# Kernel tuning notes

Hardware: AMD Instinct MI355X
Metric: run time of the kernel (lower is better)

## Reference

```python
import jax, jax.numpy as jnp
import numpy as np

N = 50000      # nodes
E = 500000     # edges
F_IN = 128     # num_features
H = 128        # hidden_dim
G = 256        # graphs in batch


def setup_inputs() -> dict:
    key = jax.random.key(0)
    ks = jax.random.split(key, 12)
    x = jax.random.normal(ks[0], (N, F_IN), jnp.float32)
    edge_index = jax.random.randint(ks[1], (2, E), 0, N, dtype=jnp.int32)
    edge_attr = jax.random.uniform(ks[2], (E,), jnp.float32)  # positive edge weights
    batch = jnp.sort(jax.random.randint(ks[3], (N,), 0, G, dtype=jnp.int32))
    s_in = 1.0 / np.sqrt(F_IN)
    s_h = 1.0 / np.sqrt(H)
    return {
        "x": x,
        "edge_index": edge_index,
        "edge_attr": edge_attr,
        "batch": batch,
        "W1": jax.random.normal(ks[4], (H, F_IN), jnp.float32) * s_in,
        "b1": jnp.zeros((H,), jnp.float32),
        "W2": jax.random.normal(ks[5], (H, H), jnp.float32) * s_h,
        "b2": jnp.zeros((H,), jnp.float32),
        "fW1": jax.random.normal(ks[6], (H, H), jnp.float32) * s_h,
        "fb1": jnp.zeros((H,), jnp.float32),
        "fW2": jax.random.normal(ks[7], (1, H), jnp.float32) * s_h,
        "fb2": jnp.zeros((1,), jnp.float32),
    }


def gcn_conv(x, src, dst, ew, W, b, n):
    """PyG GCNConv: linear transform, add self-loops (weight 1),
    symmetric deg^-1/2 normalization with edge weights, scatter-add, bias."""
    h = x @ W.T                                   # [n, H]
    loop = jnp.arange(n, dtype=src.dtype)
    s = jnp.concatenate([src, loop])
    d = jnp.concatenate([dst, loop])
    w = jnp.concatenate([ew, jnp.ones((n,), x.dtype)])
    deg = jax.ops.segment_sum(w, d, num_segments=n)  # weighted in-degree incl. self-loop
    dinv = jnp.where(deg > 0, jax.lax.rsqrt(deg), 0.0)
    norm = dinv[s] * w * dinv[d]                  # [E+n]
    msg = h[s] * norm[:, None]                    # gather + scale: [E+n, H]
    out = jax.ops.segment_sum(msg, d, num_segments=n)  # scatter-add
    return out + b


def reference(x, edge_index, edge_attr, batch, W1, b1, W2, b2, fW1, fb1, fW2, fb2):
    src, dst = edge_index[0], edge_index[1]
    h = jax.nn.relu(gcn_conv(x, src, dst, edge_attr, W1, b1, N))
    h = jax.nn.relu(gcn_conv(h, src, dst, edge_attr, W2, b2, N))
    # global_mean_pool over graph ids
    sums = jax.ops.segment_sum(h, batch, num_segments=G)            # [G, H]
    counts = jax.ops.segment_sum(jnp.ones((N,), h.dtype), batch, num_segments=G)
    pooled = sums / jnp.maximum(counts, 1.0)[:, None]
    o = jax.nn.relu(pooled @ fW1.T + fb1)
    return o @ fW2.T + fb2                                          # [G, 1]
```

## Files before the change

kernel.cpp:

```cpp
#include <hip/hip_runtime.h>
#include <hip/hip_bf16.h>


#define CAP 64
#define CDS 8

typedef __attribute__((ext_vector_type(8))) short short8;
typedef __attribute__((ext_vector_type(4))) float floatx4;

__device__ inline unsigned short f2bf(float f) {
    unsigned int u = __float_as_uint(f);
    u += 0x7FFF + ((u >> 16) & 1);
    return (unsigned short)(u >> 16);
}
__device__ inline float bf2f(unsigned short h) {
    return __uint_as_float(((unsigned int)h) << 16);
}

#define PW 136
__global__ __launch_bounds__(256) void gemm1_build(const float* __restrict__ X,
        const float* __restrict__ W, unsigned short* __restrict__ C, int M,
        const int* __restrict__ src, const int* __restrict__ dst,
        const float* __restrict__ ew, unsigned long long* __restrict__ cd,
        unsigned int* __restrict__ csr, int E, int gemmB) {
    if ((int)blockIdx.x >= gemmB) {
        int i = ((int)blockIdx.x - gemmB) * 256 + (int)threadIdx.x;
        if (i < E) {
            int d = dst[i];
            float w = ew[i];
            unsigned long long pk = (1ULL << 32) |
                                    (unsigned long long)__float2uint_rn(w * 16777216.0f);
            unsigned long long old = atomicAdd(&cd[(size_t)d * CDS], pk);
            int pos = (int)(old >> 32);
            if (pos < CAP)
                csr[((size_t)d << 6) + pos] =
                    ((unsigned int)src[i] << 16) | __float2uint_rn(w * 65535.0f);
        }
        return;
    }

    __shared__ unsigned short whi[128 * PW];
    __shared__ unsigned short wlo[128 * PW];
    const int t = threadIdx.x;

    {
        int j = t >> 1;
        int c0 = (t & 1) * 64;
        const floatx4* wr = (const floatx4*)(W + (size_t)j * 128 + c0);
        unsigned short* dh = &whi[j * PW + c0];
        unsigned short* dl = &wlo[j * PW + c0];
#pragma unroll
        for (int i = 0; i < 16; ++i) {
            floatx4 v = wr[i];
            ushort4 hv, lv;
            hv.x = f2bf(v.x); lv.x = f2bf(v.x - bf2f(hv.x));
            hv.y = f2bf(v.y); lv.y = f2bf(v.y - bf2f(hv.y));
            hv.z = f2bf(v.z); lv.z = f2bf(v.z - bf2f(hv.z));
            hv.w = f2bf(v.w); lv.w = f2bf(v.w - bf2f(hv.w));
            *(ushort4*)(dh + i * 4) = hv;
            *(ushort4*)(dl + i * 4) = lv;
        }
    }
    __syncthreads();

    const int wave = t >> 6;
    const int lane = t & 63;
    const int q = lane >> 4;
    const int ln = lane & 15;
    const int rowbase = blockIdx.x * 128 + wave * 32;

    floatx4 acc[2][8];
#pragma unroll
    for (int s = 0; s < 2; ++s)
#pragma unroll
        for (int ct = 0; ct < 8; ++ct) acc[s][ct] = (floatx4){0.f, 0.f, 0.f, 0.f};

#pragma unroll
    for (int ks = 0; ks < 4; ++ks) {
        short8 ahi[2], alo[2];
#pragma unroll
        for (int s = 0; s < 2; ++s) {
            int row = rowbase + s * 16 + ln;
            int rowc = (row < M) ? row : (M - 1);
            const floatx4* xr = (const floatx4*)(X + (size_t)rowc * 128 + ks * 32 + q * 8);
            floatx4 x0 = xr[0];
            floatx4 x1 = xr[1];
            unsigned short h, l;
            h = f2bf(x0.x); l = f2bf(x0.x - bf2f(h)); ahi[s][0] = (short)h; alo[s][0] = (short)l;
            h = f2bf(x0.y); l = f2bf(x0.y - bf2f(h)); ahi[s][1] = (short)h; alo[s][1] = (short)l;
            h = f2bf(x0.z); l = f2bf(x0.z - bf2f(h)); ahi[s][2] = (short)h; alo[s][2] = (short)l;
            h = f2bf(x0.w); l = f2bf(x0.w - bf2f(h)); ahi[s][3] = (short)h; alo[s][3] = (short)l;
            h = f2bf(x1.x); l = f2bf(x1.x - bf2f(h)); ahi[s][4] = (short)h; alo[s][4] = (short)l;
            h = f2bf(x1.y); l = f2bf(x1.y - bf2f(h)); ahi[s][5] = (short)h; alo[s][5] = (short)l;
            h = f2bf(x1.z); l = f2bf(x1.z - bf2f(h)); ahi[s][6] = (short)h; alo[s][6] = (short)l;
            h = f2bf(x1.w); l = f2bf(x1.w - bf2f(h)); ahi[s][7] = (short)h; alo[s][7] = (short)l;
        }
#pragma unroll
        for (int ct = 0; ct < 8; ++ct) {
            int lidx = (ct * 16 + ln) * PW + ks * 32 + q * 8;
            short8 bhi = *(const short8*)&whi[lidx];
            short8 blo = *(const short8*)&wlo[lidx];
#pragma unroll
            for (int s = 0; s < 2; ++s) {
                acc[s][ct] = __builtin_amdgcn_mfma_f32_16x16x32_bf16(ahi[s], bhi, acc[s][ct], 0, 0, 0);
                acc[s][ct] = __builtin_amdgcn_mfma_f32_16x16x32_bf16(ahi[s], blo, acc[s][ct], 0, 0, 0);
                acc[s][ct] = __builtin_amdgcn_mfma_f32_16x16x32_bf16(alo[s], bhi, acc[s][ct], 0, 0, 0);
            }
        }
    }

#pragma unroll
    for (int s = 0; s < 2; ++s) {
#pragma unroll
        for (int r = 0; r < 4; ++r) {
            int row = rowbase + s * 16 + q * 4 + r;
            if (row < M) {
                unsigned short* cr = C + (size_t)row * 128 + ln;
#pragma unroll
                for (int ct = 0; ct < 8; ++ct) cr[ct * 16] = f2bf(acc[s][ct][r]);
            }
        }
    }
}

__global__ __launch_bounds__(256) void compute_dinv(const unsigned long long* __restrict__ cd,
        float* __restrict__ dinv, int n) {
    int i = blockIdx.x * 256 + threadIdx.x;
    if (i < n) {
        unsigned int lo = (unsigned int)cd[(size_t)i * CDS];
        dinv[i] = rsqrtf((float)lo * 5.9604644775e-8f + 1.0f);
    }
}

__global__ __launch_bounds__(256) void gemm_bf16_nt(const unsigned short* __restrict__ X,
        const float* __restrict__ W, unsigned short* __restrict__ C, int M) {
    __shared__ unsigned short whi[128 * PW];
    __shared__ unsigned short wlo[128 * PW];
    const int t = threadIdx.x;

    {
        int j = t >> 1;
        int c0 = (t & 1) * 64;
        const floatx4* wr = (const floatx4*)(W + (size_t)j * 128 + c0);
        unsigned short* dh = &whi[j * PW + c0];
        unsigned short* dl = &wlo[j * PW + c0];
#pragma unroll
        for (int i = 0; i < 16; ++i) {
            floatx4 v = wr[i];
            ushort4 hv, lv;
            hv.x = f2bf(v.x); lv.x = f2bf(v.x - bf2f(hv.x));
            hv.y = f2bf(v.y); lv.y = f2bf(v.y - bf2f(hv.y));
            hv.z = f2bf(v.z); lv.z = f2bf(v.z - bf2f(hv.z));
            hv.w = f2bf(v.w); lv.w = f2bf(v.w - bf2f(hv.w));
            *(ushort4*)(dh + i * 4) = hv;
            *(ushort4*)(dl + i * 4) = lv;
        }
    }
    __syncthreads();

    const int wave = t >> 6;
    const int lane = t & 63;
    const int q = lane >> 4;
    const int ln = lane & 15;
    const int rowbase = blockIdx.x * 128 + wave * 32;

    floatx4 acc[2][8];
#pragma unroll
    for (int s = 0; s < 2; ++s)
#pragma unroll
        for (int ct = 0; ct < 8; ++ct) acc[s][ct] = (floatx4){0.f, 0.f, 0.f, 0.f};

#pragma unroll
    for (int ks = 0; ks < 4; ++ks) {
        short8 a[2];
#pragma unroll
        for (int s = 0; s < 2; ++s) {
            int row = rowbase + s * 16 + ln;
            int rowc = (row < M) ? row : (M - 1);
            a[s] = *(const short8*)(X + (size_t)rowc * 128 + ks * 32 + q * 8);
        }
#pragma unroll
        for (int ct = 0; ct < 8; ++ct) {
            int lidx = (ct * 16 + ln) * PW + ks * 32 + q * 8;
            short8 bhi = *(const short8*)&whi[lidx];
            short8 blo = *(const short8*)&wlo[lidx];
#pragma unroll
            for (int s = 0; s < 2; ++s) {
                acc[s][ct] = __builtin_amdgcn_mfma_f32_16x16x32_bf16(a[s], bhi, acc[s][ct], 0, 0, 0);
                acc[s][ct] = __builtin_amdgcn_mfma_f32_16x16x32_bf16(a[s], blo, acc[s][ct], 0, 0, 0);
            }
        }
    }

#pragma unroll
    for (int s = 0; s < 2; ++s) {
#pragma unroll
        for (int r = 0; r < 4; ++r) {
            int row = rowbase + s * 16 + q * 4 + r;
            if (row < M) {
                unsigned short* cr = C + (size_t)row * 128 + ln;
#pragma unroll
                for (int ct = 0; ct < 8; ++ct) cr[ct * 16] = f2bf(acc[s][ct][r]);
            }
        }
    }
}

#define UNPACK_W(e) ((float)((e) & 0xFFFFu) * (1.0f / 65535.0f))

#define FMA8(hv_, wt_)                                        \
    acc0[0] += bf2f((unsigned short)hv_[0]) * wt_;            \
    acc0[1] += bf2f((unsigned short)hv_[1]) * wt_;            \
    acc0[2] += bf2f((unsigned short)hv_[2]) * wt_;            \
    acc0[3] += bf2f((unsigned short)hv_[3]) * wt_;            \
    acc1[0] += bf2f((unsigned short)hv_[4]) * wt_;            \
    acc1[1] += bf2f((unsigned short)hv_[5]) * wt_;            \
    acc1[2] += bf2f((unsigned short)hv_[6]) * wt_;            \
    acc1[3] += bf2f((unsigned short)hv_[7]) * wt_;

__global__ __launch_bounds__(256) void aggregate_finalize(
        const unsigned short* __restrict__ h, const unsigned short* __restrict__ hlin,
        const unsigned long long* __restrict__ cd, const unsigned int* __restrict__ csr,
        const float* __restrict__ dinv, const float* __restrict__ bias,
        unsigned short* __restrict__ outb, int n) {
    int node = blockIdx.x * 16 + (threadIdx.x >> 4);
    if (node >= n) return;
    int lane = threadIdx.x & 15;
    float di = dinv[node];
    float sl = di * di;
    const floatx4* bp = (const floatx4*)bias + lane * 2;
    floatx4 b40 = bp[0];
    floatx4 b41 = bp[1];
    short8 bse = ((const short8*)(hlin + (size_t)node * 128))[lane];
    floatx4 acc0 = (floatx4){0.f, 0.f, 0.f, 0.f};
    floatx4 acc1 = (floatx4){0.f, 0.f, 0.f, 0.f};

    const unsigned int* b = csr + ((size_t)node << 6);
    const uint4* bv = (const uint4*)b;
    int c = (int)(cd[(size_t)node * CDS] >> 32);
    if (c > CAP) c = CAP;
    int k = 0;
    for (; k + 4 <= c; k += 4) {
        uint4 ev = bv[k >> 2];
        int s0 = ev.x >> 16, s1 = ev.y >> 16, s2 = ev.z >> 16, s3 = ev.w >> 16;
        float w0 = UNPACK_W(ev.x) * dinv[s0];
        float w1 = UNPACK_W(ev.y) * dinv[s1];
        float w2 = UNPACK_W(ev.z) * dinv[s2];
        float w3 = UNPACK_W(ev.w) * dinv[s3];
        short8 h0 = ((const short8*)(h + (size_t)s0 * 128))[lane];
        short8 h1 = ((const short8*)(h + (size_t)s1 * 128))[lane];
        short8 h2 = ((const short8*)(h + (size_t)s2 * 128))[lane];
        short8 h3 = ((const short8*)(h + (size_t)s3 * 128))[lane];
        FMA8(h0, w0); FMA8(h1, w1); FMA8(h2, w2); FMA8(h3, w3);
    }
    for (; k < c; ++k) {
        unsigned int e0 = b[k];
        int s0 = e0 >> 16;
        float w0 = UNPACK_W(e0) * dinv[s0];
        short8 hv = ((const short8*)(h + (size_t)s0 * 128))[lane];
        FMA8(hv, w0);
    }
    short8 o;
    o[0] = (short)f2bf(fmaxf(acc0[0] * di + bf2f((unsigned short)bse[0]) * sl + b40[0], 0.0f));
    o[1] = (short)f2bf(fmaxf(acc0[1] * di + bf2f((unsigned short)bse[1]) * sl + b40[1], 0.0f));
    o[2] = (short)f2bf(fmaxf(acc0[2] * di + bf2f((unsigned short)bse[2]) * sl + b40[2], 0.0f));
    o[3] = (short)f2bf(fmaxf(acc0[3] * di + bf2f((unsigned short)bse[3]) * sl + b40[3], 0.0f));
    o[4] = (short)f2bf(fmaxf(acc1[0] * di + bf2f((unsigned short)bse[4]) * sl + b41[0], 0.0f));
    o[5] = (short)f2bf(fmaxf(acc1[1] * di + bf2f((unsigned short)bse[5]) * sl + b41[1], 0.0f));
    o[6] = (short)f2bf(fmaxf(acc1[2] * di + bf2f((unsigned short)bse[6]) * sl + b41[2], 0.0f));
    o[7] = (short)f2bf(fmaxf(acc1[3] * di + bf2f((unsigned short)bse[7]) * sl + b41[3], 0.0f));
    ((short8*)(outb + (size_t)node * 128))[lane] = o;
}

__global__ __launch_bounds__(256) void aggregate_pool(
        const unsigned short* __restrict__ h,
        const unsigned long long* __restrict__ cd, const unsigned int* __restrict__ csr,
        const float* __restrict__ dinv, const float* __restrict__ bias,
        const int* __restrict__ batch, float* __restrict__ pooled, int n) {
    int slot = threadIdx.x >> 4;
    int node = blockIdx.x * 16 + slot;
    int lane = threadIdx.x & 15;
    __shared__ float red[16][128];
    __shared__ int grp[16];

    floatx4 r0 = (floatx4){0.f, 0.f, 0.f, 0.f};
    floatx4 r1 = (floatx4){0.f, 0.f, 0.f, 0.f};
    int g = -1;
    if (node < n) {
        g = batch[node];
        float di = dinv[node];
        float sl = di * di;
        const floatx4* bp = (const floatx4*)bias + lane * 2;
        floatx4 b40 = bp[0];
        floatx4 b41 = bp[1];
        short8 bse = ((const short8*)(h + (size_t)node * 128))[lane];
        floatx4 acc0 = (floatx4){0.f, 0.f, 0.f, 0.f};
        floatx4 acc1 = (floatx4){0.f, 0.f, 0.f, 0.f};

        const unsigned int* b = csr + ((size_t)node << 6);
        const uint4* bv = (const uint4*)b;
        int c = (int)(cd[(size_t)node * CDS] >> 32);
        if (c > CAP) c = CAP;
        int k = 0;
        for (; k + 4 <= c; k += 4) {
            uint4 ev = bv[k >> 2];
            int s0 = ev.x >> 16, s1 = ev.y >> 16, s2 = ev.z >> 16, s3 = ev.w >> 16;
            float w0 = UNPACK_W(ev.x) * dinv[s0];
            float w1 = UNPACK_W(ev.y) * dinv[s1];
            float w2 = UNPACK_W(ev.z) * dinv[s2];
            float w3 = UNPACK_W(ev.w) * dinv[s3];
            short8 h0 = ((const short8*)(h + (size_t)s0 * 128))[lane];
            short8 h1 = ((const short8*)(h + (size_t)s1 * 128))[lane];
            short8 h2 = ((const short8*)(h + (size_t)s2 * 128))[lane];
            short8 h3 = ((const short8*)(h + (size_t)s3 * 128))[lane];
            FMA8(h0, w0); FMA8(h1, w1); FMA8(h2, w2); FMA8(h3, w3);
        }
        for (; k < c; ++k) {
            unsigned int e0 = b[k];
            int s0 = e0 >> 16;
            float w0 = UNPACK_W(e0) * dinv[s0];
            short8 hv = ((const short8*)(h + (size_t)s0 * 128))[lane];
            FMA8(hv, w0);
        }
        r0[0] = fmaxf(acc0[0] * di + bf2f((unsigned short)bse[0]) * sl + b40[0], 0.0f);
        r0[1] = fmaxf(acc0[1] * di + bf2f((unsigned short)bse[1]) * sl + b40[1], 0.0f);
        r0[2] = fmaxf(acc0[2] * di + bf2f((unsigned short)bse[2]) * sl + b40[2], 0.0f);
        r0[3] = fmaxf(acc0[3] * di + bf2f((unsigned short)bse[3]) * sl + b40[3], 0.0f);
        r1[0] = fmaxf(acc1[0] * di + bf2f((unsigned short)bse[4]) * sl + b41[0], 0.0f);
        r1[1] = fmaxf(acc1[1] * di + bf2f((unsigned short)bse[5]) * sl + b41[1], 0.0f);
        r1[2] = fmaxf(acc1[2] * di + bf2f((unsigned short)bse[6]) * sl + b41[2], 0.0f);
        r1[3] = fmaxf(acc1[3] * di + bf2f((unsigned short)bse[7]) * sl + b41[3], 0.0f);
    }
    if (lane == 0) grp[slot] = g;
    *(floatx4*)&red[slot][lane * 8] = r0;
    *(floatx4*)&red[slot][lane * 8 + 4] = r1;
    __syncthreads();

    if (threadIdx.x < 128) {
        int j = threadIdx.x;
        float s = 0.f;
        int cg = -1;
#pragma unroll
        for (int r = 0; r < 16; ++r) {
            int gr = grp[r];
            if (gr != cg) {
                if (cg >= 0) atomicAdd(&pooled[(size_t)cg * 128 + j], s);
                s = 0.f;
                cg = gr;
            }
            if (gr >= 0) s += red[r][j];
        }
        if (cg >= 0) atomicAdd(&pooled[(size_t)cg * 128 + j], s);
    }
}

__global__ __launch_bounds__(128) void head_mlp(const float* __restrict__ pooled,
        const int* __restrict__ batch, int n,
        const float* __restrict__ fW1, const float* __restrict__ fb1,
        const float* __restrict__ fW2, const float* __restrict__ fb2,
        float* __restrict__ out) {
    int g = blockIdx.x;
    int j = threadIdx.x;
    int lo = 0, hi = n;
    while (lo < hi) { int mid = (lo + hi) >> 1; if (batch[mid] < g) lo = mid + 1; else hi = mid; }
    int s = lo;
    hi = n;
    while (lo < hi) { int mid = (lo + hi) >> 1; if (batch[mid] < g + 1) lo = mid + 1; else hi = mid; }
    int cnt = lo - s;
    float scale = 1.0f / fmaxf((float)cnt, 1.0f);

    __shared__ float row[128];
    __shared__ float part[2];
    row[j] = pooled[(size_t)g * 128 + j] * scale;
    __syncthreads();
    float acc = fb1[j];
    const float* wr = fW1 + (size_t)j * 128;
#pragma unroll 8
    for (int k = 0; k < 128; ++k) acc += row[k] * wr[k];
    float v = fmaxf(acc, 0.0f) * fW2[j];
#pragma unroll
    for (int off = 32; off > 0; off >>= 1) v += __shfl_down(v, off);
    if ((j & 63) == 0) part[j >> 6] = v;
    __syncthreads();
    if (j == 0) out[g] = part[0] + part[1] + fb2[0];
}

extern "C" void kernel_launch(void* const* d_in, const int* in_sizes, int n_in,
                              void* d_out, int out_size, void* d_ws, size_t ws_size,
                              hipStream_t stream) {
    const float* x   = (const float*)d_in[0];
    const int*   ei  = (const int*)d_in[1];
    const float* ew  = (const float*)d_in[2];
    const int* batch = (const int*)d_in[3];
    const float* W1  = (const float*)d_in[4];
    const float* b1  = (const float*)d_in[5];
    const float* W2  = (const float*)d_in[6];
    const float* b2  = (const float*)d_in[7];
    const float* fW1 = (const float*)d_in[8];
    const float* fb1 = (const float*)d_in[9];
    const float* fW2 = (const float*)d_in[10];
    const float* fb2 = (const float*)d_in[11];
    float* out = (float*)d_out;

    const int N = in_sizes[0] / 128;
    const int E = in_sizes[2];
    const int G = out_size;
    const int* src = ei;
    const int* dst = ei + E;

    unsigned short* A = (unsigned short*)d_ws;
    unsigned short* B = A + (size_t)N * 128;
    unsigned int* csr = (unsigned int*)(B + (size_t)N * 128);
    unsigned long long* cd = (unsigned long long*)(csr + (size_t)N * CAP);
    float* pooled = (float*)(cd + (size_t)N * CDS);
    float* dinv = pooled + (size_t)G * 128;

    const int gemmB = (N + 127) / 128;
    const int buildB = (E + 255) / 256;

    hipMemsetAsync(cd, 0, (size_t)N * CDS * 8 + (size_t)G * 128 * 4, stream);

    gemm1_build<<<gemmB + buildB, 256, 0, stream>>>(x, W1, A, N, src, dst, ew,
                                                    cd, csr, E, gemmB);
    compute_dinv<<<(N + 255) / 256, 256, 0, stream>>>(cd, dinv, N);
    aggregate_finalize<<<(N + 15) / 16, 256, 0, stream>>>(A, A, cd, csr, dinv, b1, B, N);

    gemm_bf16_nt<<<(N + 127) / 128, 256, 0, stream>>>(B, W2, A, N);
    aggregate_pool<<<(N + 15) / 16, 256, 0, stream>>>(A, cd, csr, dinv, b2, batch, pooled, N);

    head_mlp<<<G, 128, 0, stream>>>(pooled, batch, N, fW1, fb1, fW2, fb2, out);
}
```

Measured before the change: 199.8 us.

## Fuse dinv+aggregate and aggregate+pool+head into cooperative persistent kernels

Replaces the compute_dinv and aggregate_finalize launches with one cooperative persistent kernel that computes dinv, does a grid-wide sync, and then aggregates layer 1 over tiles in a grid-stride loop. It also merges aggregate_pool and head_mlp into a second cooperative kernel that ends with a grid sync followed by the per-graph MLP head. This removes two kernel launches and their gaps. In exchange it adds grid barrier costs, occupancy-limited persistent grids, and an extra __syncthreads per tile in the pooling loop.

```diff
diff --git a/kernel.cpp b/kernel.cpp
--- a/kernel.cpp
+++ b/kernel.cpp
@@ -1,9 +1,13 @@
 #include <hip/hip_runtime.h>
 #include <hip/hip_bf16.h>
-
+#include <hip/hip_cooperative_groups.h>
+
+
+namespace cg = cooperative_groups;
 
 #define CAP 64
 #define CDS 8
+#define PW 136
 
 typedef __attribute__((ext_vector_type(8))) short short8;
 typedef __attribute__((ext_vector_type(4))) float floatx4;
@@ -17,7 +21,6 @@
     return __uint_as_float(((unsigned int)h) << 16);
 }
 
-#define PW 136
 __global__ __launch_bounds__(256) void gemm1_build(const float* __restrict__ X,
         const float* __restrict__ W, unsigned short* __restrict__ C, int M,
         const int* __restrict__ src, const int* __restrict__ dst,
@@ -123,15 +126,6 @@
     }
 }
 
-__global__ __launch_bounds__(256) void compute_dinv(const unsigned long long* __restrict__ cd,
-        float* __restrict__ dinv, int n) {
-    int i = blockIdx.x * 256 + threadIdx.x;
-    if (i < n) {
-        unsigned int lo = (unsigned int)cd[(size_t)i * CDS];
-        dinv[i] = rsqrtf((float)lo * 5.9604644775e-8f + 1.0f);
-    }
-}
-
 __global__ __launch_bounds__(256) void gemm_bf16_nt(const unsigned short* __restrict__ X,
         const float* __restrict__ W, unsigned short* __restrict__ C, int M) {
     __shared__ unsigned short whi[128 * PW];
@@ -218,82 +212,29 @@
     acc1[2] += bf2f((unsigned short)hv_[6]) * wt_;            \
     acc1[3] += bf2f((unsigned short)hv_[7]) * wt_;
 
-__global__ __launch_bounds__(256) void aggregate_finalize(
+__global__ __launch_bounds__(256) void coop_dinv_agg1(
         const unsigned short* __restrict__ h, const unsigned short* __restrict__ hlin,
         const unsigned long long* __restrict__ cd, const unsigned int* __restrict__ csr,
-        const float* __restrict__ dinv, const float* __restrict__ bias,
+        float* __restrict__ dinv, const float* __restrict__ bias,
         unsigned short* __restrict__ outb, int n) {
-    int node = blockIdx.x * 16 + (threadIdx.x >> 4);
-    if (node >= n) return;
-    int lane = threadIdx.x & 15;
-    float di = dinv[node];
-    float sl = di * di;
-    const floatx4* bp = (const floatx4*)bias + lane * 2;
-    floatx4 b40 = bp[0];
-    floatx4 b41 = bp[1];
-    short8 bse = ((const short8*)(hlin + (size_t)node * 128))[lane];
-    floatx4 acc0 = (floatx4){0.f, 0.f, 0.f, 0.f};
-    floatx4 acc1 = (floatx4){0.f, 0.f, 0.f, 0.f};
-
-    const unsigned int* b = csr + ((size_t)node << 6);
-    const uint4* bv = (const uint4*)b;
-    int c = (int)(cd[(size_t)node * CDS] >> 32);
-    if (c > CAP) c = CAP;
-    int k = 0;
-    for (; k + 4 <= c; k += 4) {
-        uint4 ev = bv[k >> 2];
-        int s0 = ev.x >> 16, s1 = ev.y >> 16, s2 = ev.z >> 16, s3 = ev.w >> 16;
-        float w0 = UNPACK_W(ev.x) * dinv[s0];
-        float w1 = UNPACK_W(ev.y) * dinv[s1];
-        float w2 = UNPACK_W(ev.z) * dinv[s2];
-        float w3 = UNPACK_W(ev.w) * dinv[s3];
-        short8 h0 = ((const short8*)(h + (size_t)s0 * 128))[lane];
-        short8 h1 = ((const short8*)(h + (size_t)s1 * 128))[lane];
-        short8 h2 = ((const short8*)(h + (size_t)s2 * 128))[lane];
-        short8 h3 = ((const short8*)(h + (size_t)s3 * 128))[lane];
-        FMA8(h0, w0); FMA8(h1, w1); FMA8(h2, w2); FMA8(h3, w3);
-    }
-    for (; k < c; ++k) {
-        unsigned int e0 = b[k];
-        int s0 = e0 >> 16;
-        float w0 = UNPACK_W(e0) * dinv[s0];
-        short8 hv = ((const short8*)(h + (size_t)s0 * 128))[lane];
-        FMA8(hv, w0);
-    }
-    short8 o;
-    o[0] = (short)f2bf(fmaxf(acc0[0] * di + bf2f((unsigned short)bse[0]) * sl + b40[0], 0.0f));
-    o[1] = (short)f2bf(fmaxf(acc0[1] * di + bf2f((unsigned short)bse[1]) * sl + b40[1], 0.0f));
-    o[2] = (short)f2bf(fmaxf(acc0[2] * di + bf2f((unsigned short)bse[2]) * sl + b40[2], 0.0f));
-    o[3] = (short)f2bf(fmaxf(acc0[3] * di + bf2f((unsigned short)bse[3]) * sl + b40[3], 0.0f));
-    o[4] = (short)f2bf(fmaxf(acc1[0] * di + bf2f((unsigned short)bse[4]) * sl + b41[0], 0.0f));
-    o[5] = (short)f2bf(fmaxf(acc1[1] * di + bf2f((unsigned short)bse[5]) * sl + b41[1], 0.0f));
-    o[6] = (short)f2bf(fmaxf(acc1[2] * di + bf2f((unsigned short)bse[6]) * sl + b41[2], 0.0f));
-    o[7] = (short)f2bf(fmaxf(acc1[3] * di + bf2f((unsigned short)bse[7]) * sl + b41[3], 0.0f));
-    ((short8*)(outb + (size_t)node * 128))[lane] = o;
-}
-
-__global__ __launch_bounds__(256) void aggregate_pool(
-        const unsigned short* __restrict__ h,
-        const unsigned long long* __restrict__ cd, const unsigned int* __restrict__ csr,
-        const float* __restrict__ dinv, const float* __restrict__ bias,
-        const int* __restrict__ batch, float* __restrict__ pooled, int n) {
-    int slot = threadIdx.x >> 4;
-    int node = blockIdx.x * 16 + slot;
-    int lane = threadIdx.x & 15;
-    __shared__ float red[16][128];
-    __shared__ int grp[16];
-
-    floatx4 r0 = (floatx4){0.f, 0.f, 0.f, 0.f};
-    floatx4 r1 = (floatx4){0.f, 0.f, 0.f, 0.f};
-    int g = -1;
-    if (node < n) {
-        g = batch[node];
+    for (int i = blockIdx.x * 256 + threadIdx.x; i < n; i += gridDim.x * 256) {
+        unsigned int lo = (unsigned int)cd[(size_t)i * CDS];
+        dinv[i] = rsqrtf((float)lo * 5.9604644775e-8f + 1.0f);
+    }
+    cg::this_grid().sync();
+
+    const int slot = threadIdx.x >> 4;
+    const int lane = threadIdx.x & 15;
+    const int ntiles = (n + 15) >> 4;
+    for (int tile = blockIdx.x; tile < ntiles; tile += gridDim.x) {
+        int node = tile * 16 + slot;
+        if (node >= n) continue;
         float di = dinv[node];
         float sl = di * di;
         const floatx4* bp = (const floatx4*)bias + lane * 2;
         floatx4 b40 = bp[0];
         floatx4 b41 = bp[1];
-        short8 bse = ((const short8*)(h + (size_t)node * 128))[lane];
+        short8 bse = ((const short8*)(hlin + (size_t)node * 128))[lane];
         floatx4 acc0 = (floatx4){0.f, 0.f, 0.f, 0.f};
         floatx4 acc1 = (floatx4){0.f, 0.f, 0.f, 0.f};
 
@@ -322,67 +263,137 @@
             short8 hv = ((const short8*)(h + (size_t)s0 * 128))[lane];
             FMA8(hv, w0);
         }
-        r0[0] = fmaxf(acc0[0] * di + bf2f((unsigned short)bse[0]) * sl + b40[0], 0.0f);
-        r0[1] = fmaxf(acc0[1] * di + bf2f((unsigned short)bse[1]) * sl + b40[1], 0.0f);
-        r0[2] = fmaxf(acc0[2] * di + bf2f((unsigned short)bse[2]) * sl + b40[2], 0.0f);
-        r0[3] = fmaxf(acc0[3] * di + bf2f((unsigned short)bse[3]) * sl + b40[3], 0.0f);
-        r1[0] = fmaxf(acc1[0] * di + bf2f((unsigned short)bse[4]) * sl + b41[0], 0.0f);
-        r1[1] = fmaxf(acc1[1] * di + bf2f((unsigned short)bse[5]) * sl + b41[1], 0.0f);
-        r1[2] = fmaxf(acc1[2] * di + bf2f((unsigned short)bse[6]) * sl + b41[2], 0.0f);
-        r1[3] = fmaxf(acc1[3] * di + bf2f((unsigned short)bse[7]) * sl + b41[3], 0.0f);
-    }
-    if (lane == 0) grp[slot] = g;
-    *(floatx4*)&red[slot][lane * 8] = r0;
-    *(floatx4*)&red[slot][lane * 8 + 4] = r1;
-    __syncthreads();
-
-    if (threadIdx.x < 128) {
-        int j = threadIdx.x;
-        float s = 0.f;
-        int cg = -1;
-#pragma unroll
-        for (int r = 0; r < 16; ++r) {
-            int gr = grp[r];
-            if (gr != cg) {
-                if (cg >= 0) atomicAdd(&pooled[(size_t)cg * 128 + j], s);
-                s = 0.f;
-                cg = gr;
-            }
-            if (gr >= 0) s += red[r][j];
-        }
-        if (cg >= 0) atomicAdd(&pooled[(size_t)cg * 128 + j], s);
-    }
-}
-
-__global__ __launch_bounds__(128) void head_mlp(const float* __restrict__ pooled,
-        const int* __restrict__ batch, int n,
+        short8 o;
+        o[0] = (short)f2bf(fmaxf(acc0[0] * di + bf2f((unsigned short)bse[0]) * sl + b40[0], 0.0f));
+        o[1] = (short)f2bf(fmaxf(acc0[1] * di + bf2f((unsigned short)bse[1]) * sl + b40[1], 0.0f));
+        o[2] = (short)f2bf(fmaxf(acc0[2] * di + bf2f((unsigned short)bse[2]) * sl + b40[2], 0.0f));
+        o[3] = (short)f2bf(fmaxf(acc0[3] * di + bf2f((unsigned short)bse[3]) * sl + b40[3], 0.0f));
+        o[4] = (short)f2bf(fmaxf(acc1[0] * di + bf2f((unsigned short)bse[4]) * sl + b41[0], 0.0f));
+        o[5] = (short)f2bf(fmaxf(acc1[1] * di + bf2f((unsigned short)bse[5]) * sl + b41[1], 0.0f));
+        o[6] = (short)f2bf(fmaxf(acc1[2] * di + bf2f((unsigned short)bse[6]) * sl + b41[2], 0.0f));
+        o[7] = (short)f2bf(fmaxf(acc1[3] * di + bf2f((unsigned short)bse[7]) * sl + b41[3], 0.0f));
+        ((short8*)(outb + (size_t)node * 128))[lane] = o;
+    }
+}
+
+__global__ __launch_bounds__(256) void coop_aggpool_head(
+        const unsigned short* __restrict__ h,
+        const unsigned long long* __restrict__ cd, const unsigned int* __restrict__ csr,
+        const float* __restrict__ dinv, const float* __restrict__ bias,
+        const int* __restrict__ batch, float* __restrict__ pooled, int n,
         const float* __restrict__ fW1, const float* __restrict__ fb1,
         const float* __restrict__ fW2, const float* __restrict__ fb2,
-        float* __restrict__ out) {
-    int g = blockIdx.x;
-    int j = threadIdx.x;
-    int lo = 0, hi = n;
-    while (lo < hi) { int mid = (lo + hi) >> 1; if (batch[mid] < g) lo = mid + 1; else hi = mid; }
-    int s = lo;
-    hi = n;
-    while (lo < hi) { int mid = (lo + hi) >> 1; if (batch[mid] < g + 1) lo = mid + 1; else hi = mid; }
-    int cnt = lo - s;
-    float scale = 1.0f / fmaxf((float)cnt, 1.0f);
-
-    __shared__ float row[128];
-    __shared__ float part[2];
-    row[j] = pooled[(size_t)g * 128 + j] * scale;
-    __syncthreads();
-    float acc = fb1[j];
-    const float* wr = fW1 + (size_t)j * 128;
+        float* __restrict__ out, int G) {
+    __shared__ float red[16][128];
+    __shared__ int grp[16];
+    const int slot = threadIdx.x >> 4;
+    const int lane = threadIdx.x & 15;
+    const int ntiles = (n + 15) >> 4;
+
+    for (int tile = blockIdx.x; tile < ntiles; tile += gridDim.x) {
+        int node = tile * 16 + slot;
+        floatx4 r0 = (floatx4){0.f, 0.f, 0.f, 0.f};
+        floatx4 r1 = (floatx4){0.f, 0.f, 0.f, 0.f};
+        int g = -1;
+        if (node < n) {
+            g = batch[node];
+            float di = dinv[node];
+            float sl = di * di;
+            const floatx4* bp = (const floatx4*)bias + lane * 2;
+            floatx4 b40 = bp[0];
+            floatx4 b41 = bp[1];
+            short8 bse = ((const short8*)(h + (size_t)node * 128))[lane];
+            floatx4 acc0 = (floatx4){0.f, 0.f, 0.f, 0.f};
+            floatx4 acc1 = (floatx4){0.f, 0.f, 0.f, 0.f};
+
+            const unsigned int* b = csr + ((size_t)node << 6);
+            const uint4* bv = (const uint4*)b;
+            int c = (int)(cd[(size_t)node * CDS] >> 32);
+            if (c > CAP) c = CAP;
+            int k = 0;
+            for (; k + 4 <= c; k += 4) {
+                uint4 ev = bv[k >> 2];
+                int s0 = ev.x >> 16, s1 = ev.y >> 16, s2 = ev.z >> 16, s3 = ev.w >> 16;
+                float w0 = UNPACK_W(ev.x) * dinv[s0];
+                float w1 = UNPACK_W(ev.y) * dinv[s1];
+                float w2 = UNPACK_W(ev.z) * dinv[s2];
+                float w3 = UNPACK_W(ev.w) * dinv[s3];
+                short8 h0 = ((const short8*)(h + (size_t)s0 * 128))[lane];
+                short8 h1 = ((const short8*)(h + (size_t)s1 * 128))[lane];
+                short8 h2 = ((const short8*)(h + (size_t)s2 * 128))[lane];
+                short8 h3 = ((const short8*)(h + (size_t)s3 * 128))[lane];
+                FMA8(h0, w0); FMA8(h1, w1); FMA8(h2, w2); FMA8(h3, w3);
+            }
+            for (; k < c; ++k) {
+                unsigned int e0 = b[k];
+                int s0 = e0 >> 16;
+                float w0 = UNPACK_W(e0) * dinv[s0];
+                short8 hv = ((const short8*)(h + (size_t)s0 * 128))[lane];
+                FMA8(hv, w0);
+            }
+            r0[0] = fmaxf(acc0[0] * di + bf2f((unsigned short)bse[0]) * sl + b40[0], 0.0f);
+            r0[1] = fmaxf(acc0[1] * di + bf2f((unsigned short)bse[1]) * sl + b40[1], 0.0f);
+            r0[2] = fmaxf(acc0[2] * di + bf2f((unsigned short)bse[2]) * sl + b40[2], 0.0f);
+            r0[3] = fmaxf(acc0[3] * di + bf2f((unsigned short)bse[3]) * sl + b40[3], 0.0f);
+            r1[0] = fmaxf(acc1[0] * di + bf2f((unsigned short)bse[4]) * sl + b41[0], 0.0f);
+            r1[1] = fmaxf(acc1[1] * di + bf2f((unsigned short)bse[5]) * sl + b41[1], 0.0f);
+            r1[2] = fmaxf(acc1[2] * di + bf2f((unsigned short)bse[6]) * sl + b41[2], 0.0f);
+            r1[3] = fmaxf(acc1[3] * di + bf2f((unsigned short)bse[7]) * sl + b41[3], 0.0f);
+        }
+        if (lane == 0) grp[slot] = g;
+        *(floatx4*)&red[slot][lane * 8] = r0;
+        *(floatx4*)&red[slot][lane * 8 + 4] = r1;
+        __syncthreads();
+
+        if (threadIdx.x < 128) {
+            int j = threadIdx.x;
+            float s = 0.f;
+            int cg2 = -1;
+#pragma unroll
+            for (int r = 0; r < 16; ++r) {
+                int gr = grp[r];
+                if (gr != cg2) {
+                    if (cg2 >= 0) atomicAdd(&pooled[(size_t)cg2 * 128 + j], s);
+                    s = 0.f;
+                    cg2 = gr;
+                }
+                if (gr >= 0) s += red[r][j];
+            }
+            if (cg2 >= 0) atomicAdd(&pooled[(size_t)cg2 * 128 + j], s);
+        }
+        __syncthreads();
+    }
+
+    cg::this_grid().sync();
+
+    if ((int)blockIdx.x < G) {
+        int g = blockIdx.x;
+        int j = threadIdx.x;
+        int lo = 0, hi = n;
+        while (lo < hi) { int mid = (lo + hi) >> 1; if (batch[mid] < g) lo = mid + 1; else hi = mid; }
+        int s = lo;
+        hi = n;
+        while (lo < hi) { int mid = (lo + hi) >> 1; if (batch[mid] < g + 1) lo = mid + 1; else hi = mid; }
+        int cnt = lo - s;
+        float scale = 1.0f / fmaxf((float)cnt, 1.0f);
+
+        __shared__ float row[128];
+        __shared__ float part[2];
+        if (j < 128) row[j] = pooled[(size_t)g * 128 + j] * scale;
+        __syncthreads();
+        if (j < 128) {
+            float acc = fb1[j];
+            const float* wr = fW1 + (size_t)j * 128;
 #pragma unroll 8
-    for (int k = 0; k < 128; ++k) acc += row[k] * wr[k];
-    float v = fmaxf(acc, 0.0f) * fW2[j];
-#pragma unroll
-    for (int off = 32; off > 0; off >>= 1) v += __shfl_down(v, off);
-    if ((j & 63) == 0) part[j >> 6] = v;
-    __syncthreads();
-    if (j == 0) out[g] = part[0] + part[1] + fb2[0];
+            for (int k = 0; k < 128; ++k) acc += row[k] * wr[k];
+            float v = fmaxf(acc, 0.0f) * fW2[j];
+#pragma unroll
+            for (int off = 32; off > 0; off >>= 1) v += __shfl_down(v, off);
+            if ((j & 63) == 0) part[j >> 6] = v;
+        }
+        __syncthreads();
+        if (j == 0) out[g] = part[0] + part[1] + fb2[0];
+    }
 }
 
 extern "C" void kernel_launch(void* const* d_in, const int* in_sizes, int n_in,
@@ -422,11 +433,41 @@
 
     gemm1_build<<<gemmB + buildB, 256, 0, stream>>>(x, W1, A, N, src, dst, ew,
                                                     cd, csr, E, gemmB);
-    compute_dinv<<<(N + 255) / 256, 256, 0, stream>>>(cd, dinv, N);
-    aggregate_finalize<<<(N + 15) / 16, 256, 0, stream>>>(A, A, cd, csr, dinv, b1, B, N);
+
+    {
+        int maxb = 0;
+        if (hipOccupancyMaxActiveBlocksPerMultiprocessor(&maxb, coop_dinv_agg1, 256, 0)
+                != hipSuccess || maxb < 1) maxb = 4;
+        int grid = maxb * 256;
+        if (grid > 2048) grid = 2048;
+        if (grid < 256) grid = 256;
+        const unsigned short* hA = A;
+        const unsigned short* hlinA = A;
+        unsigned short* outB = B;
+        int n_ = N;
+        void* args[] = {(void*)&hA, (void*)&hlinA, (void*)&cd, (void*)&csr,
+                        (void*)&dinv, (void*)&b1, (void*)&outB, (void*)&n_};
+        hipLaunchCooperativeKernel((void*)coop_dinv_agg1, dim3(grid), dim3(256),
+                                   args, 0, stream);
+    }
 
     gemm_bf16_nt<<<(N + 127) / 128, 256, 0, stream>>>(B, W2, A, N);
-    aggregate_pool<<<(N + 15) / 16, 256, 0, stream>>>(A, cd, csr, dinv, b2, batch, pooled, N);
-
-    head_mlp<<<G, 128, 0, stream>>>(pooled, batch, N, fW1, fb1, fW2, fb2, out);
-}
+
+    {
+        int maxb = 0;
+        if (hipOccupancyMaxActiveBlocksPerMultiprocessor(&maxb, coop_aggpool_head, 256, 0)
+                != hipSuccess || maxb < 1) maxb = 4;
+        int grid = maxb * 256;
+        if (grid > 2048) grid = 2048;
+        if (grid < 256) grid = 256;
+        const unsigned short* hA = A;
+        int n_ = N;
+        int g_ = G;
+        void* args[] = {(void*)&hA, (void*)&cd, (void*)&csr, (void*)&dinv,
+                        (void*)&b2, (void*)&batch, (void*)&pooled, (void*)&n_,
+                        (void*)&fW1, (void*)&fb1, (void*)&fW2, (void*)&fb2,
+                        (void*)&out, (void*)&g_};
+        hipLaunchCooperativeKernel((void*)coop_aggpool_head, dim3(grid), dim3(256),
+                                   args, 0, stream);
+    }
+}
```

New measurement: 363.4 us. +81.9%, slower.
